# Kernel optimization log

Hardware: AMD Instinct MI355X
Metric: run time of the kernel (lower is better)

The kernel has to match this reference:

```python
import jax, jax.numpy as jnp
import numpy as np

EPS = 1e-8
B, L, D = 8, 2048, 128

def _l2norm(x):
    # F.normalize-style: x / max(||x||, eps)
    n = jnp.sqrt(jnp.sum(x * x, axis=-1, keepdims=True))
    return x / jnp.maximum(n, EPS)

def setup_inputs() -> dict:
    key = jax.random.key(0)
    k0, k1, k2, k3, k4 = jax.random.split(key, 5)
    context = jax.random.normal(k0, (B, 2, L, D), dtype=jnp.float32)
    # MlpModule (BLINK-style): Linear(D, D) -> ReLU -> Linear(D, 1)
    W1 = jax.random.normal(k1, (D, D), dtype=jnp.float32) * (1.0 / np.sqrt(D))
    b1 = jnp.zeros((D,), dtype=jnp.float32)
    W2 = jax.random.normal(k2, (D, 1), dtype=jnp.float32) * (1.0 / np.sqrt(D))
    b2 = jnp.zeros((1,), dtype=jnp.float32)
    return {"context": context, "W1": W1, "b1": b1, "W2": W2, "b2": b2}

def reference(context, W1, b1, W2, b2):
    ctx = context[:, 0]          # [B, L, D] mention-side tokens
    ent = context[:, 1]          # [B, L, D] entity-side tokens
    cn = _l2norm(ctx)
    en = _l2norm(ent)
    # cosine similarity matrix [B, L, L]
    sim = jnp.einsum("bld,bmd->blm", cn, en)
    idx = jnp.argmax(sim, axis=-1)                          # [B, L]
    matched = jnp.take_along_axis(en, idx[..., None], axis=1)  # [B, L, D]
    pair = jnp.stack([cn, matched], axis=-2)                # [B, L, 2, D]
    h = jax.nn.relu(pair @ W1 + b1)                         # [B, L, 2, D]
    out = h @ W2 + b2                                       # [B, L, 2, 1]
    return jnp.sum(out, axis=-2).squeeze(-1)                # [B, L]
```

## Files before the change

### kernel.cpp

```cpp
#include <hip/hip_runtime.h>
#include <hip/hip_bf16.h>

#define B_ 8
#define L_ 2048
#define D_ 128
#define BL_ (B_ * L_)
#define DELTA2 0.016f
#define QCAP 4096

typedef __attribute__((ext_vector_type(8))) short bf16x8;
typedef __attribute__((ext_vector_type(4))) float f32x4;

__global__ void k_norm(const float* __restrict__ ctx,
                       float* __restrict__ cn, float* __restrict__ en,
                       ushort* __restrict__ cnb, ushort* __restrict__ enb) {
    int wid  = blockIdx.x * 4 + (threadIdx.x >> 6);
    int lane = threadIdx.x & 63;
    int b   = wid >> 12;
    int rem = wid & 4095;
    int c   = rem >> 11;
    int l   = rem & 2047;

    const float* src = ctx + (size_t)wid * D_;
    float2 v = ((const float2*)src)[lane];
    float ss = v.x * v.x + v.y * v.y;
    #pragma unroll
    for (int off = 32; off; off >>= 1) ss += __shfl_down(ss, off, 64);
    ss = __shfl(ss, 0, 64);
    float n = fmaxf(sqrtf(ss), 1e-8f);
    float ox = v.x / n, oy = v.y / n;

    size_t ro = (size_t)(b * L_ + l) * D_;
    float* dst = (c == 0 ? cn : en) + ro;
    ((float2*)dst)[lane] = make_float2(ox, oy);

    __hip_bfloat16 hx = __float2bfloat16(ox), hy = __float2bfloat16(oy);
    ushort ux = *(ushort*)&hx, uy = *(ushort*)&hy;
    ushort* dstb = (c == 0 ? cnb : enb) + ro;
    ((ushort2*)dstb)[lane] = make_ushort2(ux, uy);
}

__device__ __forceinline__ void tile64(const bf16x8* __restrict__ Areg,
                                       const ushort* __restrict__ Bb,
                                       int m, int q, f32x4 acc[4][4]) {
    #pragma unroll
    for (int rt = 0; rt < 4; ++rt)
        #pragma unroll
        for (int ct = 0; ct < 4; ++ct) acc[rt][ct] = (f32x4){0.f, 0.f, 0.f, 0.f};
    #pragma unroll
    for (int kc = 0; kc < 4; ++kc) {
        bf16x8 bfrag[4];
        #pragma unroll
        for (int ct = 0; ct < 4; ++ct)
            bfrag[ct] = *(const bf16x8*)(Bb + (size_t)(ct * 16 + m) * D_ + kc * 32 + q * 8);
        #pragma unroll
        for (int rt = 0; rt < 4; ++rt)
            #pragma unroll
            for (int ct = 0; ct < 4; ++ct)
                acc[rt][ct] = __builtin_amdgcn_mfma_f32_16x16x32_bf16(
                    Areg[rt * 4 + kc], bfrag[ct], acc[rt][ct], 0, 0, 0);
    }
}

__global__ __launch_bounds__(512) void k_sim(const ushort* __restrict__ cnb,
                                             const ushort* __restrict__ enb,
                                             const float* __restrict__ cn,
                                             const float* __restrict__ en,
                                             int* __restrict__ finalidx) {
    __shared__ float wrowmax[8][64];
    __shared__ float rowth_l[64];
    __shared__ unsigned long long bestw[8][64];
    __shared__ int qbuf[QCAP];
    __shared__ int qn;

    int bid = blockIdx.x;
    int b = bid & 7, rb = bid >> 3;
    int row0 = rb * 64;
    int tid = threadIdx.x;
    int wave = tid >> 6, lane = tid & 63;
    int m = lane & 15, q = lane >> 4;

    if (tid == 0) qn = 0;
    bestw[wave][lane] = 0ULL;

    const ushort* Ab  = cnb + ((size_t)(b * L_) + row0) * D_;
    const ushort* Bb0 = enb + (size_t)(b * L_) * D_;

    bf16x8 Areg[16];
    #pragma unroll
    for (int rt = 0; rt < 4; ++rt)
        #pragma unroll
        for (int kc = 0; kc < 4; ++kc)
            Areg[rt * 4 + kc] = *(const bf16x8*)(Ab + (size_t)(rt * 16 + m) * D_ + kc * 32 + q * 8);

    float runmax[16];
    #pragma unroll
    for (int s = 0; s < 16; ++s) runmax[s] = -3.0e38f;

    for (int t = 0; t < 4; ++t) {
        f32x4 acc[4][4];
        tile64(Areg, Bb0 + (size_t)(wave * 256 + t * 64) * D_, m, q, acc);
        #pragma unroll
        for (int rt = 0; rt < 4; ++rt)
            #pragma unroll
            for (int reg = 0; reg < 4; ++reg) {
                float v = fmaxf(fmaxf(acc[rt][0][reg], acc[rt][1][reg]),
                                fmaxf(acc[rt][2][reg], acc[rt][3][reg]));
                runmax[rt * 4 + reg] = fmaxf(runmax[rt * 4 + reg], v);
            }
    }
    #pragma unroll
    for (int s = 0; s < 16; ++s) {
        float v = runmax[s];
        v = fmaxf(v, __shfl_xor(v, 1, 64));
        v = fmaxf(v, __shfl_xor(v, 2, 64));
        v = fmaxf(v, __shfl_xor(v, 4, 64));
        v = fmaxf(v, __shfl_xor(v, 8, 64));
        runmax[s] = v;
    }
    if (m == 0) {
        #pragma unroll
        for (int rt = 0; rt < 4; ++rt)
            #pragma unroll
            for (int reg = 0; reg < 4; ++reg)
                wrowmax[wave][rt * 16 + q * 4 + reg] = runmax[rt * 4 + reg];
    }
    __syncthreads();
    if (tid < 64) {
        float rm = wrowmax[0][tid];
        #pragma unroll
        for (int w = 1; w < 8; ++w) rm = fmaxf(rm, wrowmax[w][tid]);
        rowth_l[tid] = rm - DELTA2;
    }
    __syncthreads();
    float rowth_r[16];
    #pragma unroll
    for (int rt = 0; rt < 4; ++rt)
        #pragma unroll
        for (int reg = 0; reg < 4; ++reg)
            rowth_r[rt * 4 + reg] = rowth_l[rt * 16 + q * 4 + reg];

    for (int t = 0; t < 4; ++t) {
        int col0 = wave * 256 + t * 64;
        f32x4 acc[4][4];
        tile64(Areg, Bb0 + (size_t)col0 * D_, m, q, acc);
        #pragma unroll
        for (int rt = 0; rt < 4; ++rt)
            #pragma unroll
            for (int reg = 0; reg < 4; ++reg) {
                float th = rowth_r[rt * 4 + reg];
                float mx = fmaxf(fmaxf(acc[rt][0][reg], acc[rt][1][reg]),
                                 fmaxf(acc[rt][2][reg], acc[rt][3][reg]));
                if (mx >= th) {
                    #pragma unroll
                    for (int ct = 0; ct < 4; ++ct)
                        if (acc[rt][ct][reg] >= th) {
                            int pos = atomicAdd(&qn, 1);
                            if (pos < QCAP)
                                qbuf[pos] = ((rt * 16 + q * 4 + reg) << 12) |
                                            (col0 + ct * 16 + m);
                        }
                }
            }
    }
    __syncthreads();

    int qtot = min(qn, QCAP);
    for (int e = wave; e < qtot; e += 8) {
        int pc = qbuf[e];
        int rl = pc >> 12, col = pc & 0xFFF;
        const float* ar = cn + ((size_t)(b * L_) + row0 + rl) * D_;
        const float* br = en + ((size_t)(b * L_) + col) * D_;
        float2 x = ((const float2*)ar)[lane];
        float2 y = ((const float2*)br)[lane];
        double s = (double)x.x * y.x + (double)x.y * y.y;
        #pragma unroll
        for (int off = 32; off; off >>= 1) s += __shfl_down(s, off, 64);
        if (lane == 0) {
            unsigned long long ub = (unsigned long long)__double_as_longlong(s);
            ub = (ub & 0x8000000000000000ULL) ? ~ub : (ub | 0x8000000000000000ULL);
            ub = (ub & ~0x7FFULL) | (unsigned long long)(2047 - col);
            if (ub > bestw[wave][rl]) bestw[wave][rl] = ub;
        }
    }
    __syncthreads();
    if (tid < 64) {
        unsigned long long bb = bestw[0][tid];
        #pragma unroll
        for (int w = 1; w < 8; ++w) { unsigned long long t2 = bestw[w][tid]; if (t2 > bb) bb = t2; }
        finalidx[b * L_ + row0 + tid] = 2047 - (int)(bb & 0x7FFULL);
    }
}

__global__ __launch_bounds__(256) void k_feval(
        const float* __restrict__ X,
        const float* __restrict__ W1, const float* __restrict__ b1,
        const float* __restrict__ W2, const float* __restrict__ b2,
        float* __restrict__ g) {
    __shared__ __align__(16) float As[32][132];
    __shared__ __align__(16) float Bs[32][132];
    __shared__ float redv[128][16];

    int tid = threadIdx.x;
    int tx = tid & 15, ty = tid >> 4;
    int r  = tid >> 3, kg = tid & 7;
    int row0 = blockIdx.x * 128;
    const float* Ab = X + (size_t)row0 * D_;

    float acc[8][8];
    #pragma unroll
    for (int i = 0; i < 8; ++i)
        #pragma unroll
        for (int j = 0; j < 8; ++j) acc[i][j] = 0.0f;

    for (int kc = 0; kc < 4; ++kc) {
        __syncthreads();
        #pragma unroll
        for (int p = 0; p < 4; ++p) {
            int rr = r + 32 * p;
            float4 v = *(const float4*)(Ab + (size_t)rr * D_ + kc * 32 + kg * 4);
            As[kg][rr]      = v.x;
            As[8 + kg][rr]  = v.y;
            As[16 + kg][rr] = v.z;
            As[24 + kg][rr] = v.w;
        }
        {
            int kr = r, phys = (kr & 3) * 8 + (kr >> 2);
            const float* srcp = W1 + (size_t)(kc * 32 + kr) * D_ + kg * 16;
            #pragma unroll
            for (int qq = 0; qq < 4; ++qq)
                *(float4*)&Bs[phys][kg * 16 + qq * 4] = *(const float4*)(srcp + qq * 4);
        }
        __syncthreads();
        #pragma unroll
        for (int k = 0; k < 32; ++k) {
            float a[8], bb[8];
            *(float4*)&a[0]  = *(const float4*)&As[k][ty * 4];
            *(float4*)&a[4]  = *(const float4*)&As[k][64 + ty * 4];
            *(float4*)&bb[0] = *(const float4*)&Bs[k][tx * 4];
            *(float4*)&bb[4] = *(const float4*)&Bs[k][64 + tx * 4];
            #pragma unroll
            for (int i = 0; i < 8; ++i)
                #pragma unroll
                for (int j = 0; j < 8; ++j)
                    acc[i][j] = fmaf(a[i], bb[j], acc[i][j]);
        }
    }

    float w2j[8], b1j[8];
    #pragma unroll
    for (int jj = 0; jj < 8; ++jj) {
        int c = (jj < 4) ? (tx * 4 + jj) : (64 + tx * 4 + (jj - 4));
        w2j[jj] = W2[c];
        b1j[jj] = b1[c];
    }
    float bias2 = b2[0];
    __syncthreads();
    #pragma unroll
    for (int i = 0; i < 8; ++i) {
        float s = 0.0f;
        #pragma unroll
        for (int jj = 0; jj < 8; ++jj)
            s += fmaxf(acc[i][jj] + b1j[jj], 0.0f) * w2j[jj];
        int rowl = (i < 4) ? (ty * 4 + i) : (64 + ty * 4 + (i - 4));
        redv[rowl][tx] = s;
    }
    __syncthreads();
    if (tid < 128) {
        float s = 0.0f;
        #pragma unroll
        for (int tt = 0; tt < 16; ++tt) s += redv[tid][tt];
        g[row0 + tid] = s + bias2;
    }
}

__global__ void k_out(const int* __restrict__ finalidx,
                      const float* __restrict__ g, float* __restrict__ out) {
    int rr = blockIdx.x * 256 + threadIdx.x;
    if (rr >= BL_) return;
    int b = rr >> 11;
    out[rr] = g[rr] + g[BL_ + (b << 11) + finalidx[rr]];
}

extern "C" void kernel_launch(void* const* d_in, const int* in_sizes, int n_in,
                              void* d_out, int out_size, void* d_ws, size_t ws_size,
                              hipStream_t stream) {
    const float* context = (const float*)d_in[0];
    const float* W1 = (const float*)d_in[1];
    const float* b1 = (const float*)d_in[2];
    const float* W2 = (const float*)d_in[3];
    const float* b2 = (const float*)d_in[4];
    float* out = (float*)d_out;

    char* ws = (char*)d_ws;
    float*  cn  = (float*)(ws);
    float*  en  = (float*)(ws + 8388608);
    ushort* cnb = (ushort*)(ws + 16777216);
    ushort* enb = (ushort*)(ws + 20971520);
    float*  g   = (float*)(ws + 25165824);
    int* finalidx = (int*)(ws + 25296896);

    k_norm<<<8192, 256, 0, stream>>>(context, cn, en, cnb, enb);
    k_sim<<<256, 512, 0, stream>>>(cnb, enb, cn, en, finalidx);
    k_feval<<<256, 256, 0, stream>>>(cn, W1, b1, W2, b2, g);
    k_out<<<BL_ / 256, 256, 0, stream>>>(finalidx, g, out);
}
```

Baseline: 146.2 us.

## Fuse k_sim into single GEMM pass with running-max candidate filter, halve row tiles

The similarity kernel no longer computes the bf16 GEMM twice. It does one pass with a running per-wave row maximum, queues candidates against that evolving threshold with their approximate scores stored in 64-bit entries, and filters them against the final block-wide threshold before the fp64 refinement. Row tiles shrink from 64 to 32 (k_sim) and from 128 to 64 (k_feval), doubling the grid sizes for more parallelism and occupancy. The cost is a larger queue footprint and more candidates early in the pass, when the threshold is still loose, which could hit QCAP overflow or add refinement work.

```diff
diff --git a/kernel.cpp b/kernel.cpp
--- a/kernel.cpp
+++ b/kernel.cpp
@@ -7,6 +7,7 @@
 #define BL_ (B_ * L_)
 #define DELTA2 0.016f
 #define QCAP 4096
+#define ROWS 32
 
 typedef __attribute__((ext_vector_type(8))) short bf16x8;
 typedef __attribute__((ext_vector_type(4))) float f32x4;
@@ -40,151 +41,133 @@
     ((ushort2*)dstb)[lane] = make_ushort2(ux, uy);
 }
 
-__device__ __forceinline__ void tile64(const bf16x8* __restrict__ Areg,
-                                       const ushort* __restrict__ Bb,
-                                       int m, int q, f32x4 acc[4][4]) {
-    #pragma unroll
-    for (int rt = 0; rt < 4; ++rt)
-        #pragma unroll
-        for (int ct = 0; ct < 4; ++ct) acc[rt][ct] = (f32x4){0.f, 0.f, 0.f, 0.f};
-    #pragma unroll
-    for (int kc = 0; kc < 4; ++kc) {
-        bf16x8 bfrag[4];
-        #pragma unroll
-        for (int ct = 0; ct < 4; ++ct)
-            bfrag[ct] = *(const bf16x8*)(Bb + (size_t)(ct * 16 + m) * D_ + kc * 32 + q * 8);
-        #pragma unroll
-        for (int rt = 0; rt < 4; ++rt)
-            #pragma unroll
-            for (int ct = 0; ct < 4; ++ct)
-                acc[rt][ct] = __builtin_amdgcn_mfma_f32_16x16x32_bf16(
-                    Areg[rt * 4 + kc], bfrag[ct], acc[rt][ct], 0, 0, 0);
-    }
-}
-
-__global__ __launch_bounds__(512) void k_sim(const ushort* __restrict__ cnb,
-                                             const ushort* __restrict__ enb,
-                                             const float* __restrict__ cn,
-                                             const float* __restrict__ en,
-                                             int* __restrict__ finalidx) {
-    __shared__ float wrowmax[8][64];
-    __shared__ float rowth_l[64];
-    __shared__ unsigned long long bestw[8][64];
-    __shared__ int qbuf[QCAP];
+__global__ __launch_bounds__(512, 4) void k_sim(const ushort* __restrict__ cnb,
+                                                const ushort* __restrict__ enb,
+                                                const float* __restrict__ cn,
+                                                const float* __restrict__ en,
+                                                int* __restrict__ finalidx) {
+    __shared__ float wrowmax[8][ROWS];
+    __shared__ float rowth_l[ROWS];
+    __shared__ unsigned long long bestw[8][ROWS];
+    __shared__ unsigned long long qbuf[QCAP];
     __shared__ int qn;
 
     int bid = blockIdx.x;
     int b = bid & 7, rb = bid >> 3;
-    int row0 = rb * 64;
+    int row0 = rb * ROWS;
     int tid = threadIdx.x;
     int wave = tid >> 6, lane = tid & 63;
     int m = lane & 15, q = lane >> 4;
 
     if (tid == 0) qn = 0;
-    bestw[wave][lane] = 0ULL;
+    if (lane < ROWS) bestw[wave][lane] = 0ULL;
+    __syncthreads();
 
     const ushort* Ab  = cnb + ((size_t)(b * L_) + row0) * D_;
     const ushort* Bb0 = enb + (size_t)(b * L_) * D_;
 
-    bf16x8 Areg[16];
-    #pragma unroll
-    for (int rt = 0; rt < 4; ++rt)
+    bf16x8 Areg[8];
+    #pragma unroll
+    for (int rt = 0; rt < 2; ++rt)
         #pragma unroll
         for (int kc = 0; kc < 4; ++kc)
             Areg[rt * 4 + kc] = *(const bf16x8*)(Ab + (size_t)(rt * 16 + m) * D_ + kc * 32 + q * 8);
 
-    float runmax[16];
-    #pragma unroll
-    for (int s = 0; s < 16; ++s) runmax[s] = -3.0e38f;
-
-    for (int t = 0; t < 4; ++t) {
-        f32x4 acc[4][4];
-        tile64(Areg, Bb0 + (size_t)(wave * 256 + t * 64) * D_, m, q, acc);
-        #pragma unroll
-        for (int rt = 0; rt < 4; ++rt)
-            #pragma unroll
-            for (int reg = 0; reg < 4; ++reg) {
-                float v = fmaxf(fmaxf(acc[rt][0][reg], acc[rt][1][reg]),
-                                fmaxf(acc[rt][2][reg], acc[rt][3][reg]));
-                runmax[rt * 4 + reg] = fmaxf(runmax[rt * 4 + reg], v);
-            }
-    }
-    #pragma unroll
-    for (int s = 0; s < 16; ++s) {
-        float v = runmax[s];
-        v = fmaxf(v, __shfl_xor(v, 1, 64));
-        v = fmaxf(v, __shfl_xor(v, 2, 64));
-        v = fmaxf(v, __shfl_xor(v, 4, 64));
-        v = fmaxf(v, __shfl_xor(v, 8, 64));
-        runmax[s] = v;
-    }
-    if (m == 0) {
-        #pragma unroll
-        for (int rt = 0; rt < 4; ++rt)
-            #pragma unroll
-            for (int reg = 0; reg < 4; ++reg)
-                wrowmax[wave][rt * 16 + q * 4 + reg] = runmax[rt * 4 + reg];
-    }
-    __syncthreads();
-    if (tid < 64) {
-        float rm = wrowmax[0][tid];
-        #pragma unroll
-        for (int w = 1; w < 8; ++w) rm = fmaxf(rm, wrowmax[w][tid]);
-        rowth_l[tid] = rm - DELTA2;
-    }
-    __syncthreads();
-    float rowth_r[16];
-    #pragma unroll
-    for (int rt = 0; rt < 4; ++rt)
-        #pragma unroll
-        for (int reg = 0; reg < 4; ++reg)
-            rowth_r[rt * 4 + reg] = rowth_l[rt * 16 + q * 4 + reg];
+    float runmax[8];
+    #pragma unroll
+    for (int s = 0; s < 8; ++s) runmax[s] = -3.0e38f;
 
     for (int t = 0; t < 4; ++t) {
         int col0 = wave * 256 + t * 64;
-        f32x4 acc[4][4];
-        tile64(Areg, Bb0 + (size_t)col0 * D_, m, q, acc);
-        #pragma unroll
-        for (int rt = 0; rt < 4; ++rt)
+        const ushort* Bb = Bb0 + (size_t)col0 * D_;
+
+        f32x4 acc[2][4];
+        #pragma unroll
+        for (int rt = 0; rt < 2; ++rt)
+            #pragma unroll
+            for (int ct = 0; ct < 4; ++ct) acc[rt][ct] = (f32x4){0.f, 0.f, 0.f, 0.f};
+        #pragma unroll
+        for (int kc = 0; kc < 4; ++kc) {
+            bf16x8 bfrag[4];
+            #pragma unroll
+            for (int ct = 0; ct < 4; ++ct)
+                bfrag[ct] = *(const bf16x8*)(Bb + (size_t)(ct * 16 + m) * D_ + kc * 32 + q * 8);
+            #pragma unroll
+            for (int rt = 0; rt < 2; ++rt)
+                #pragma unroll
+                for (int ct = 0; ct < 4; ++ct)
+                    acc[rt][ct] = __builtin_amdgcn_mfma_f32_16x16x32_bf16(
+                        Areg[rt * 4 + kc], bfrag[ct], acc[rt][ct], 0, 0, 0);
+        }
+
+        #pragma unroll
+        for (int rt = 0; rt < 2; ++rt)
             #pragma unroll
             for (int reg = 0; reg < 4; ++reg) {
-                float th = rowth_r[rt * 4 + reg];
-                float mx = fmaxf(fmaxf(acc[rt][0][reg], acc[rt][1][reg]),
-                                 fmaxf(acc[rt][2][reg], acc[rt][3][reg]));
-                if (mx >= th) {
+                int s = rt * 4 + reg;
+                float mx4 = fmaxf(fmaxf(acc[rt][0][reg], acc[rt][1][reg]),
+                                  fmaxf(acc[rt][2][reg], acc[rt][3][reg]));
+                float trm = mx4;
+                trm = fmaxf(trm, __shfl_xor(trm, 1, 64));
+                trm = fmaxf(trm, __shfl_xor(trm, 2, 64));
+                trm = fmaxf(trm, __shfl_xor(trm, 4, 64));
+                trm = fmaxf(trm, __shfl_xor(trm, 8, 64));
+                runmax[s] = fmaxf(runmax[s], trm);
+                float th = runmax[s] - DELTA2;
+                if (mx4 >= th) {
+                    int row = rt * 16 + q * 4 + reg;
                     #pragma unroll
                     for (int ct = 0; ct < 4; ++ct)
                         if (acc[rt][ct][reg] >= th) {
                             int pos = atomicAdd(&qn, 1);
                             if (pos < QCAP)
-                                qbuf[pos] = ((rt * 16 + q * 4 + reg) << 12) |
-                                            (col0 + ct * 16 + m);
+                                qbuf[pos] =
+                                    ((unsigned long long)__float_as_uint(acc[rt][ct][reg]) << 32) |
+                                    (unsigned)(row << 11) | (unsigned)(col0 + ct * 16 + m);
                         }
                 }
             }
     }
+
+    if (m == 0) {
+        #pragma unroll
+        for (int rt = 0; rt < 2; ++rt)
+            #pragma unroll
+            for (int reg = 0; reg < 4; ++reg)
+                wrowmax[wave][rt * 16 + q * 4 + reg] = runmax[rt * 4 + reg];
+    }
+    __syncthreads();
+    if (tid < ROWS) {
+        float rm = wrowmax[0][tid];
+        #pragma unroll
+        for (int w = 1; w < 8; ++w) rm = fmaxf(rm, wrowmax[w][tid]);
+        rowth_l[tid] = rm - DELTA2;
+    }
     __syncthreads();
 
     int qtot = min(qn, QCAP);
     for (int e = wave; e < qtot; e += 8) {
-        int pc = qbuf[e];
-        int rl = pc >> 12, col = pc & 0xFFF;
+        unsigned long long pk = qbuf[e];
+        int rl  = (int)((pk >> 11) & 31u);
+        int col = (int)(pk & 2047u);
+        float v = __uint_as_float((unsigned)(pk >> 32));
+        if (v < rowth_l[rl]) continue;
         const float* ar = cn + ((size_t)(b * L_) + row0 + rl) * D_;
         const float* br = en + ((size_t)(b * L_) + col) * D_;
         float2 x = ((const float2*)ar)[lane];
         float2 y = ((const float2*)br)[lane];
-        double s = (double)x.x * y.x + (double)x.y * y.y;
-        #pragma unroll
-        for (int off = 32; off; off >>= 1) s += __shfl_down(s, off, 64);
+        double sdot = (double)x.x * y.x + (double)x.y * y.y;
+        #pragma unroll
+        for (int off = 32; off; off >>= 1) sdot += __shfl_down(sdot, off, 64);
         if (lane == 0) {
-            unsigned long long ub = (unsigned long long)__double_as_longlong(s);
+            unsigned long long ub = (unsigned long long)__double_as_longlong(sdot);
             ub = (ub & 0x8000000000000000ULL) ? ~ub : (ub | 0x8000000000000000ULL);
             ub = (ub & ~0x7FFULL) | (unsigned long long)(2047 - col);
             if (ub > bestw[wave][rl]) bestw[wave][rl] = ub;
         }
     }
     __syncthreads();
-    if (tid < 64) {
+    if (tid < ROWS) {
         unsigned long long bb = bestw[0][tid];
         #pragma unroll
         for (int w = 1; w < 8; ++w) { unsigned long long t2 = bestw[w][tid]; if (t2 > bb) bb = t2; }
@@ -197,26 +180,26 @@
         const float* __restrict__ W1, const float* __restrict__ b1,
         const float* __restrict__ W2, const float* __restrict__ b2,
         float* __restrict__ g) {
-    __shared__ __align__(16) float As[32][132];
+    __shared__ __align__(16) float As[32][68];
     __shared__ __align__(16) float Bs[32][132];
-    __shared__ float redv[128][16];
+    __shared__ float redv[64][16];
 
     int tid = threadIdx.x;
     int tx = tid & 15, ty = tid >> 4;
     int r  = tid >> 3, kg = tid & 7;
-    int row0 = blockIdx.x * 128;
+    int row0 = blockIdx.x * 64;
     const float* Ab = X + (size_t)row0 * D_;
 
-    float acc[8][8];
-    #pragma unroll
-    for (int i = 0; i < 8; ++i)
+    float acc[4][8];
+    #pragma unroll
+    for (int i = 0; i < 4; ++i)
         #pragma unroll
         for (int j = 0; j < 8; ++j) acc[i][j] = 0.0f;
 
     for (int kc = 0; kc < 4; ++kc) {
         __syncthreads();
         #pragma unroll
-        for (int p = 0; p < 4; ++p) {
+        for (int p = 0; p < 2; ++p) {
             int rr = r + 32 * p;
             float4 v = *(const float4*)(Ab + (size_t)rr * D_ + kc * 32 + kg * 4);
             As[kg][rr]      = v.x;
@@ -234,13 +217,12 @@
         __syncthreads();
         #pragma unroll
         for (int k = 0; k < 32; ++k) {
-            float a[8], bb[8];
+            float a[4], bb[8];
             *(float4*)&a[0]  = *(const float4*)&As[k][ty * 4];
-            *(float4*)&a[4]  = *(const float4*)&As[k][64 + ty * 4];
             *(float4*)&bb[0] = *(const float4*)&Bs[k][tx * 4];
             *(float4*)&bb[4] = *(const float4*)&Bs[k][64 + tx * 4];
             #pragma unroll
-            for (int i = 0; i < 8; ++i)
+            for (int i = 0; i < 4; ++i)
                 #pragma unroll
                 for (int j = 0; j < 8; ++j)
                     acc[i][j] = fmaf(a[i], bb[j], acc[i][j]);
@@ -257,16 +239,15 @@
     float bias2 = b2[0];
     __syncthreads();
     #pragma unroll
-    for (int i = 0; i < 8; ++i) {
+    for (int i = 0; i < 4; ++i) {
         float s = 0.0f;
         #pragma unroll
         for (int jj = 0; jj < 8; ++jj)
             s += fmaxf(acc[i][jj] + b1j[jj], 0.0f) * w2j[jj];
-        int rowl = (i < 4) ? (ty * 4 + i) : (64 + ty * 4 + (i - 4));
-        redv[rowl][tx] = s;
-    }
-    __syncthreads();
-    if (tid < 128) {
+        redv[ty * 4 + i][tx] = s;
+    }
+    __syncthreads();
+    if (tid < 64) {
         float s = 0.0f;
         #pragma unroll
         for (int tt = 0; tt < 16; ++tt) s += redv[tid][tt];
@@ -301,7 +282,7 @@
     int* finalidx = (int*)(ws + 25296896);
 
     k_norm<<<8192, 256, 0, stream>>>(context, cn, en, cnb, enb);
-    k_sim<<<256, 512, 0, stream>>>(cnb, enb, cn, en, finalidx);
-    k_feval<<<256, 256, 0, stream>>>(cn, W1, b1, W2, b2, g);
+    k_sim<<<512, 512, 0, stream>>>(cnb, enb, cn, en, finalidx);
+    k_feval<<<512, 256, 0, stream>>>(cn, W1, b1, W2, b2, g);
     k_out<<<BL_ / 256, 256, 0, stream>>>(finalidx, g, out);
 }
```

Measured after the change: 161.2 us. 1.1x slower.

## Double-buffer entity tiles into LDS via async global loads in similarity kernel

Applied to the files above, without the earlier changes.

The similarity kernel now streams entity bf16 tiles into per-wave double-buffered shared memory with global_load_lds, interleaving the column chunks across waves and overlapping loads with MFMA work through manual vmcnt waits. The candidate re-check now handles four candidates per wave at once with 16-lane reductions and a shared atomicMax, replacing the per-wave best arrays. The MLP eval kernel halves its rows per block and doubles the grid to raise parallelism. The trade-off is a large LDS footprint that may limit occupancy, plus reliance on hand-counted waitcnt values.

```diff
diff --git a/kernel.cpp b/kernel.cpp
--- a/kernel.cpp
+++ b/kernel.cpp
@@ -10,6 +10,12 @@
 
 typedef __attribute__((ext_vector_type(8))) short bf16x8;
 typedef __attribute__((ext_vector_type(4))) float f32x4;
+
+__device__ __forceinline__ void gload_lds16(const void* g, void* l) {
+    __builtin_amdgcn_global_load_lds(
+        (const __attribute__((address_space(1))) unsigned int*)g,
+        (__attribute__((address_space(3))) unsigned int*)l, 16, 0, 0);
+}
 
 __global__ void k_norm(const float* __restrict__ ctx,
                        float* __restrict__ cn, float* __restrict__ en,
@@ -40,51 +46,33 @@
     ((ushort2*)dstb)[lane] = make_ushort2(ux, uy);
 }
 
-__device__ __forceinline__ void tile64(const bf16x8* __restrict__ Areg,
-                                       const ushort* __restrict__ Bb,
-                                       int m, int q, f32x4 acc[4][4]) {
-    #pragma unroll
-    for (int rt = 0; rt < 4; ++rt)
-        #pragma unroll
-        for (int ct = 0; ct < 4; ++ct) acc[rt][ct] = (f32x4){0.f, 0.f, 0.f, 0.f};
-    #pragma unroll
-    for (int kc = 0; kc < 4; ++kc) {
-        bf16x8 bfrag[4];
-        #pragma unroll
-        for (int ct = 0; ct < 4; ++ct)
-            bfrag[ct] = *(const bf16x8*)(Bb + (size_t)(ct * 16 + m) * D_ + kc * 32 + q * 8);
-        #pragma unroll
-        for (int rt = 0; rt < 4; ++rt)
-            #pragma unroll
-            for (int ct = 0; ct < 4; ++ct)
-                acc[rt][ct] = __builtin_amdgcn_mfma_f32_16x16x32_bf16(
-                    Areg[rt * 4 + kc], bfrag[ct], acc[rt][ct], 0, 0, 0);
-    }
-}
-
-__global__ __launch_bounds__(512) void k_sim(const ushort* __restrict__ cnb,
-                                             const ushort* __restrict__ enb,
-                                             const float* __restrict__ cn,
-                                             const float* __restrict__ en,
-                                             int* __restrict__ finalidx) {
+__global__ __launch_bounds__(512, 2) void k_sim(const ushort* __restrict__ cnb,
+                                                const ushort* __restrict__ enb,
+                                                const float* __restrict__ cn,
+                                                const float* __restrict__ en,
+                                                int* __restrict__ finalidx) {
+    __shared__ char Bsm[8][2][8192];
     __shared__ float wrowmax[8][64];
     __shared__ float rowth_l[64];
-    __shared__ unsigned long long bestw[8][64];
+    __shared__ unsigned long long best[64];
     __shared__ int qbuf[QCAP];
     __shared__ int qn;
 
-    int bid = blockIdx.x;
-    int b = bid & 7, rb = bid >> 3;
-    int row0 = rb * 64;
-    int tid = threadIdx.x;
-    int wave = tid >> 6, lane = tid & 63;
-    int m = lane & 15, q = lane >> 4;
+    const int bid = blockIdx.x;
+    const int b = bid & 7, rb = bid >> 3;
+    const int row0 = rb * 64;
+    const int tid = threadIdx.x;
+    const int wave = tid >> 6, lane = tid & 63;
+    const int m = lane & 15, q = lane >> 4;
 
     if (tid == 0) qn = 0;
-    bestw[wave][lane] = 0ULL;
+    if (tid < 64) best[tid] = 0ULL;
 
     const ushort* Ab  = cnb + ((size_t)(b * L_) + row0) * D_;
     const ushort* Bb0 = enb + (size_t)(b * L_) * D_;
+    const char* gw = (const char*)Bb0 + (size_t)wave * 8192;
+    char* l0 = &Bsm[wave][0][0];
+    char* l1 = &Bsm[wave][1][0];
 
     bf16x8 Areg[16];
     #pragma unroll
@@ -93,22 +81,67 @@
         for (int kc = 0; kc < 4; ++kc)
             Areg[rt * 4 + kc] = *(const bf16x8*)(Ab + (size_t)(rt * 16 + m) * D_ + kc * 32 + q * 8);
 
+    auto STAGE = [&](int sc, char* lbuf) {
+        const char* src = gw + (size_t)sc * 65536 + (size_t)lane * 16;
+        #pragma unroll
+        for (int i = 0; i < 8; ++i)
+            gload_lds16(src + i * 1024, lbuf + i * 1024);
+    };
+    auto TILE = [&](const char* lbuf, f32x4 acc[4][2]) {
+        #pragma unroll
+        for (int rt = 0; rt < 4; ++rt)
+            #pragma unroll
+            for (int ct = 0; ct < 2; ++ct) acc[rt][ct] = (f32x4){0.f, 0.f, 0.f, 0.f};
+        #pragma unroll
+        for (int kc = 0; kc < 4; ++kc) {
+            bf16x8 bf0 = *(const bf16x8*)(lbuf + (size_t)(m) * 256 + kc * 64 + q * 16);
+            bf16x8 bf1 = *(const bf16x8*)(lbuf + (size_t)(16 + m) * 256 + kc * 64 + q * 16);
+            #pragma unroll
+            for (int rt = 0; rt < 4; ++rt) {
+                acc[rt][0] = __builtin_amdgcn_mfma_f32_16x16x32_bf16(Areg[rt * 4 + kc], bf0, acc[rt][0], 0, 0, 0);
+                acc[rt][1] = __builtin_amdgcn_mfma_f32_16x16x32_bf16(Areg[rt * 4 + kc], bf1, acc[rt][1], 0, 0, 0);
+            }
+        }
+    };
+
     float runmax[16];
     #pragma unroll
     for (int s = 0; s < 16; ++s) runmax[s] = -3.0e38f;
 
-    for (int t = 0; t < 4; ++t) {
-        f32x4 acc[4][4];
-        tile64(Areg, Bb0 + (size_t)(wave * 256 + t * 64) * D_, m, q, acc);
-        #pragma unroll
-        for (int rt = 0; rt < 4; ++rt)
-            #pragma unroll
-            for (int reg = 0; reg < 4; ++reg) {
-                float v = fmaxf(fmaxf(acc[rt][0][reg], acc[rt][1][reg]),
-                                fmaxf(acc[rt][2][reg], acc[rt][3][reg]));
-                runmax[rt * 4 + reg] = fmaxf(runmax[rt * 4 + reg], v);
-            }
-    }
+    STAGE(0, l0);
+    #pragma unroll 1
+    for (int scp = 0; scp < 4; ++scp) {
+        int sc0 = scp * 2;
+        STAGE(sc0 + 1, l1);
+        asm volatile("s_waitcnt vmcnt(8)" ::: "memory");
+        {
+            f32x4 acc[4][2];
+            TILE(l0, acc);
+            #pragma unroll
+            for (int rt = 0; rt < 4; ++rt)
+                #pragma unroll
+                for (int reg = 0; reg < 4; ++reg)
+                    runmax[rt * 4 + reg] = fmaxf(runmax[rt * 4 + reg],
+                                                 fmaxf(acc[rt][0][reg], acc[rt][1][reg]));
+        }
+        if (scp < 3) {
+            STAGE(sc0 + 2, l0);
+            asm volatile("s_waitcnt vmcnt(8)" ::: "memory");
+        } else {
+            asm volatile("s_waitcnt vmcnt(0)" ::: "memory");
+        }
+        {
+            f32x4 acc[4][2];
+            TILE(l1, acc);
+            #pragma unroll
+            for (int rt = 0; rt < 4; ++rt)
+                #pragma unroll
+                for (int reg = 0; reg < 4; ++reg)
+                    runmax[rt * 4 + reg] = fmaxf(runmax[rt * 4 + reg],
+                                                 fmaxf(acc[rt][0][reg], acc[rt][1][reg]));
+        }
+    }
+
     #pragma unroll
     for (int s = 0; s < 16; ++s) {
         float v = runmax[s];
@@ -140,56 +173,91 @@
         for (int reg = 0; reg < 4; ++reg)
             rowth_r[rt * 4 + reg] = rowth_l[rt * 16 + q * 4 + reg];
 
-    for (int t = 0; t < 4; ++t) {
-        int col0 = wave * 256 + t * 64;
-        f32x4 acc[4][4];
-        tile64(Areg, Bb0 + (size_t)col0 * D_, m, q, acc);
-        #pragma unroll
-        for (int rt = 0; rt < 4; ++rt)
-            #pragma unroll
-            for (int reg = 0; reg < 4; ++reg) {
-                float th = rowth_r[rt * 4 + reg];
-                float mx = fmaxf(fmaxf(acc[rt][0][reg], acc[rt][1][reg]),
-                                 fmaxf(acc[rt][2][reg], acc[rt][3][reg]));
-                if (mx >= th) {
-                    #pragma unroll
-                    for (int ct = 0; ct < 4; ++ct)
-                        if (acc[rt][ct][reg] >= th) {
-                            int pos = atomicAdd(&qn, 1);
-                            if (pos < QCAP)
-                                qbuf[pos] = ((rt * 16 + q * 4 + reg) << 12) |
-                                            (col0 + ct * 16 + m);
-                        }
+    STAGE(0, l0);
+    #pragma unroll 1
+    for (int scp = 0; scp < 4; ++scp) {
+        int sc0 = scp * 2;
+        STAGE(sc0 + 1, l1);
+        asm volatile("s_waitcnt vmcnt(8)" ::: "memory");
+        {
+            f32x4 acc[4][2];
+            TILE(l0, acc);
+            int col0 = sc0 * 256 + wave * 32;
+            #pragma unroll
+            for (int rt = 0; rt < 4; ++rt)
+                #pragma unroll
+                for (int reg = 0; reg < 4; ++reg) {
+                    float th = rowth_r[rt * 4 + reg];
+                    if (fmaxf(acc[rt][0][reg], acc[rt][1][reg]) >= th) {
+                        int row = rt * 16 + q * 4 + reg;
+                        #pragma unroll
+                        for (int ct = 0; ct < 2; ++ct)
+                            if (acc[rt][ct][reg] >= th) {
+                                int pos = atomicAdd(&qn, 1);
+                                if (pos < QCAP)
+                                    qbuf[pos] = (row << 12) | (col0 + ct * 16 + m);
+                            }
+                    }
                 }
-            }
+        }
+        if (scp < 3) {
+            STAGE(sc0 + 2, l0);
+            asm volatile("s_waitcnt vmcnt(8)" ::: "memory");
+        } else {
+            asm volatile("s_waitcnt vmcnt(0)" ::: "memory");
+        }
+        {
+            f32x4 acc[4][2];
+            TILE(l1, acc);
+            int col0 = (sc0 + 1) * 256 + wave * 32;
+            #pragma unroll
+            for (int rt = 0; rt < 4; ++rt)
+                #pragma unroll
+                for (int reg = 0; reg < 4; ++reg) {
+                    float th = rowth_r[rt * 4 + reg];
+                    if (fmaxf(acc[rt][0][reg], acc[rt][1][reg]) >= th) {
+                        int row = rt * 16 + q * 4 + reg;
+                        #pragma unroll
+                        for (int ct = 0; ct < 2; ++ct)
+                            if (acc[rt][ct][reg] >= th) {
+                                int pos = atomicAdd(&qn, 1);
+                                if (pos < QCAP)
+                                    qbuf[pos] = (row << 12) | (col0 + ct * 16 + m);
+                            }
+                    }
+                }
+        }
     }
     __syncthreads();
 
     int qtot = min(qn, QCAP);
-    for (int e = wave; e < qtot; e += 8) {
-        int pc = qbuf[e];
-        int rl = pc >> 12, col = pc & 0xFFF;
+    for (int e0 = wave * 4; e0 < qtot; e0 += 32) {
+        int e = e0 + q;
+        bool act = (e < qtot);
+        int pc = qbuf[act ? e : (qtot - 1)];
+        int rl = (pc >> 12) & 63, col = pc & 0xFFF;
         const float* ar = cn + ((size_t)(b * L_) + row0 + rl) * D_;
         const float* br = en + ((size_t)(b * L_) + col) * D_;
-        float2 x = ((const float2*)ar)[lane];
-        float2 y = ((const float2*)br)[lane];
-        double s = (double)x.x * y.x + (double)x.y * y.y;
-        #pragma unroll
-        for (int off = 32; off; off >>= 1) s += __shfl_down(s, off, 64);
-        if (lane == 0) {
+        float4 x0 = ((const float4*)ar)[m * 2], x1 = ((const float4*)ar)[m * 2 + 1];
+        float4 y0 = ((const float4*)br)[m * 2], y1 = ((const float4*)br)[m * 2 + 1];
+        double s = (double)x0.x * y0.x + (double)x0.y * y0.y +
+                   (double)x0.z * y0.z + (double)x0.w * y0.w +
+                   (double)x1.x * y1.x + (double)x1.y * y1.y +
+                   (double)x1.z * y1.z + (double)x1.w * y1.w;
+        s += __shfl_xor(s, 1, 64);
+        s += __shfl_xor(s, 2, 64);
+        s += __shfl_xor(s, 4, 64);
+        s += __shfl_xor(s, 8, 64);
+        if (act && m == 0) {
             unsigned long long ub = (unsigned long long)__double_as_longlong(s);
             ub = (ub & 0x8000000000000000ULL) ? ~ub : (ub | 0x8000000000000000ULL);
             ub = (ub & ~0x7FFULL) | (unsigned long long)(2047 - col);
-            if (ub > bestw[wave][rl]) bestw[wave][rl] = ub;
-        }
-    }
-    __syncthreads();
-    if (tid < 64) {
-        unsigned long long bb = bestw[0][tid];
-        #pragma unroll
-        for (int w = 1; w < 8; ++w) { unsigned long long t2 = bestw[w][tid]; if (t2 > bb) bb = t2; }
-        finalidx[b * L_ + row0 + tid] = 2047 - (int)(bb & 0x7FFULL);
-    }
+            atomicMax(&best[rl], ub);
+        }
+    }
+    __syncthreads();
+    if (tid < 64)
+        finalidx[b * L_ + row0 + tid] = 2047 - (int)(best[tid] & 0x7FFULL);
 }
 
 __global__ __launch_bounds__(256) void k_feval(
@@ -197,26 +265,26 @@
         const float* __restrict__ W1, const float* __restrict__ b1,
         const float* __restrict__ W2, const float* __restrict__ b2,
         float* __restrict__ g) {
-    __shared__ __align__(16) float As[32][132];
+    __shared__ __align__(16) float As[32][68];
     __shared__ __align__(16) float Bs[32][132];
-    __shared__ float redv[128][16];
+    __shared__ float redv[64][16];
 
     int tid = threadIdx.x;
     int tx = tid & 15, ty = tid >> 4;
     int r  = tid >> 3, kg = tid & 7;
-    int row0 = blockIdx.x * 128;
+    int row0 = blockIdx.x * 64;
     const float* Ab = X + (size_t)row0 * D_;
 
-    float acc[8][8];
-    #pragma unroll
-    for (int i = 0; i < 8; ++i)
+    float acc[4][8];
+    #pragma unroll
+    for (int i = 0; i < 4; ++i)
         #pragma unroll
         for (int j = 0; j < 8; ++j) acc[i][j] = 0.0f;
 
     for (int kc = 0; kc < 4; ++kc) {
         __syncthreads();
         #pragma unroll
-        for (int p = 0; p < 4; ++p) {
+        for (int p = 0; p < 2; ++p) {
             int rr = r + 32 * p;
             float4 v = *(const float4*)(Ab + (size_t)rr * D_ + kc * 32 + kg * 4);
             As[kg][rr]      = v.x;
@@ -234,13 +302,12 @@
         __syncthreads();
         #pragma unroll
         for (int k = 0; k < 32; ++k) {
-            float a[8], bb[8];
+            float a[4], bb[8];
             *(float4*)&a[0]  = *(const float4*)&As[k][ty * 4];
-            *(float4*)&a[4]  = *(const float4*)&As[k][64 + ty * 4];
             *(float4*)&bb[0] = *(const float4*)&Bs[k][tx * 4];
             *(float4*)&bb[4] = *(const float4*)&Bs[k][64 + tx * 4];
             #pragma unroll
-            for (int i = 0; i < 8; ++i)
+            for (int i = 0; i < 4; ++i)
                 #pragma unroll
                 for (int j = 0; j < 8; ++j)
                     acc[i][j] = fmaf(a[i], bb[j], acc[i][j]);
@@ -257,16 +324,15 @@
     float bias2 = b2[0];
     __syncthreads();
     #pragma unroll
-    for (int i = 0; i < 8; ++i) {
+    for (int i = 0; i < 4; ++i) {
         float s = 0.0f;
         #pragma unroll
         for (int jj = 0; jj < 8; ++jj)
             s += fmaxf(acc[i][jj] + b1j[jj], 0.0f) * w2j[jj];
-        int rowl = (i < 4) ? (ty * 4 + i) : (64 + ty * 4 + (i - 4));
-        redv[rowl][tx] = s;
-    }
-    __syncthreads();
-    if (tid < 128) {
+        redv[ty * 4 + i][tx] = s;
+    }
+    __syncthreads();
+    if (tid < 64) {
         float s = 0.0f;
         #pragma unroll
         for (int tt = 0; tt < 16; ++tt) s += redv[tid][tt];
@@ -302,6 +368,6 @@
 
     k_norm<<<8192, 256, 0, stream>>>(context, cn, en, cnb, enb);
     k_sim<<<256, 512, 0, stream>>>(cnb, enb, cn, en, finalidx);
-    k_feval<<<256, 256, 0, stream>>>(cn, W1, b1, W2, b2, g);
+    k_feval<<<512, 256, 0, stream>>>(cn, W1, b1, W2, b2, g);
     k_out<<<BL_ / 256, 256, 0, stream>>>(finalidx, g, out);
 }
```

After: 126.3 us. 1.16x faster.

## Stage entity tiles through LDS with async global_load_lds pipeline in k_sim

Applied to the files above, without the earlier changes.

Rewrites the similarity kernel so each wave streams its 256 entity columns in 16-column chunks into a swizzled 4-deep LDS ring via global_load_lds, with vmcnt waits to overlap loads with MFMA. The second pass walks the chunks in reverse so the last staged chunks are reused without reloading. Refinement now uses four 16-lane groups per wave for the fp64 dot products and an LDS atomicMax into a single best array instead of per-wave arrays. It adds 128KB of LDS and a launch bound of 2 blocks per CU, which may limit occupancy, and relies on hand-counted waitcnt values being correct.

```diff
diff --git a/kernel.cpp b/kernel.cpp
--- a/kernel.cpp
+++ b/kernel.cpp
@@ -10,6 +10,14 @@
 
 typedef __attribute__((ext_vector_type(8))) short bf16x8;
 typedef __attribute__((ext_vector_type(4))) float f32x4;
+
+__device__ __forceinline__ void gload_lds16(const void* g, void* l) {
+    __builtin_amdgcn_global_load_lds(
+        (const __attribute__((address_space(1))) unsigned int*)g,
+        (__attribute__((address_space(3))) unsigned int*)l, 16, 0, 0);
+}
+
+#define WAIT_VM(N) asm volatile("s_waitcnt vmcnt(" #N ")" ::: "memory")
 
 __global__ void k_norm(const float* __restrict__ ctx,
                        float* __restrict__ cn, float* __restrict__ en,
@@ -40,51 +48,31 @@
     ((ushort2*)dstb)[lane] = make_ushort2(ux, uy);
 }
 
-__device__ __forceinline__ void tile64(const bf16x8* __restrict__ Areg,
-                                       const ushort* __restrict__ Bb,
-                                       int m, int q, f32x4 acc[4][4]) {
-    #pragma unroll
-    for (int rt = 0; rt < 4; ++rt)
-        #pragma unroll
-        for (int ct = 0; ct < 4; ++ct) acc[rt][ct] = (f32x4){0.f, 0.f, 0.f, 0.f};
-    #pragma unroll
-    for (int kc = 0; kc < 4; ++kc) {
-        bf16x8 bfrag[4];
-        #pragma unroll
-        for (int ct = 0; ct < 4; ++ct)
-            bfrag[ct] = *(const bf16x8*)(Bb + (size_t)(ct * 16 + m) * D_ + kc * 32 + q * 8);
-        #pragma unroll
-        for (int rt = 0; rt < 4; ++rt)
-            #pragma unroll
-            for (int ct = 0; ct < 4; ++ct)
-                acc[rt][ct] = __builtin_amdgcn_mfma_f32_16x16x32_bf16(
-                    Areg[rt * 4 + kc], bfrag[ct], acc[rt][ct], 0, 0, 0);
-    }
-}
-
-__global__ __launch_bounds__(512) void k_sim(const ushort* __restrict__ cnb,
-                                             const ushort* __restrict__ enb,
-                                             const float* __restrict__ cn,
-                                             const float* __restrict__ en,
-                                             int* __restrict__ finalidx) {
+__global__ __launch_bounds__(512, 2) void k_sim(const ushort* __restrict__ cnb,
+                                                const ushort* __restrict__ enb,
+                                                const float* __restrict__ cn,
+                                                const float* __restrict__ en,
+                                                int* __restrict__ finalidx) {
+    __shared__ __align__(16) char Bsm[8][4][4096];
     __shared__ float wrowmax[8][64];
     __shared__ float rowth_l[64];
-    __shared__ unsigned long long bestw[8][64];
+    __shared__ unsigned long long best[64];
     __shared__ int qbuf[QCAP];
     __shared__ int qn;
 
-    int bid = blockIdx.x;
-    int b = bid & 7, rb = bid >> 3;
-    int row0 = rb * 64;
-    int tid = threadIdx.x;
-    int wave = tid >> 6, lane = tid & 63;
-    int m = lane & 15, q = lane >> 4;
+    const int bid = blockIdx.x;
+    const int b = bid & 7, rb = bid >> 3;
+    const int row0 = rb * 64;
+    const int tid = threadIdx.x;
+    const int wave = tid >> 6, lane = tid & 63;
+    const int m = lane & 15, q = lane >> 4;
 
     if (tid == 0) qn = 0;
-    bestw[wave][lane] = 0ULL;
-
-    const ushort* Ab  = cnb + ((size_t)(b * L_) + row0) * D_;
-    const ushort* Bb0 = enb + (size_t)(b * L_) * D_;
+    if (tid < 64) best[tid] = 0ULL;
+
+    const ushort* Ab = cnb + ((size_t)(b * L_) + row0) * D_;
+    const char* gw = (const char*)(enb + (size_t)(b * L_) * D_) + (size_t)wave * 65536;
+    char* Bw = &Bsm[wave][0][0];
 
     bf16x8 Areg[16];
     #pragma unroll
@@ -93,22 +81,53 @@
         for (int kc = 0; kc < 4; ++kc)
             Areg[rt * 4 + kc] = *(const bf16x8*)(Ab + (size_t)(rt * 16 + m) * D_ + kc * 32 + q * 8);
 
+    auto STAGE = [&](int c) {
+        const char* gc = gw + (size_t)c * 4096;
+        char* lbuf = Bw + (c & 3) * 4096;
+        #pragma unroll
+        for (int i = 0; i < 4; ++i) {
+            int j = i * 4 + q;
+            int so = j * 256 + ((m ^ (j & 7)) << 4);
+            gload_lds16(gc + so, lbuf + i * 1024);
+        }
+    };
+    auto TILE = [&](int c, f32x4 acc[4]) {
+        const char* lbuf = Bw + (c & 3) * 4096;
+        #pragma unroll
+        for (int rt = 0; rt < 4; ++rt) acc[rt] = (f32x4){0.f, 0.f, 0.f, 0.f};
+        #pragma unroll
+        for (int kc = 0; kc < 4; ++kc) {
+            bf16x8 bf = *(const bf16x8*)(lbuf + m * 256 + ((kc * 64 + q * 16) ^ ((m & 7) << 4)));
+            #pragma unroll
+            for (int rt = 0; rt < 4; ++rt)
+                acc[rt] = __builtin_amdgcn_mfma_f32_16x16x32_bf16(Areg[rt * 4 + kc], bf, acc[rt], 0, 0, 0);
+        }
+    };
+
     float runmax[16];
     #pragma unroll
     for (int s = 0; s < 16; ++s) runmax[s] = -3.0e38f;
 
-    for (int t = 0; t < 4; ++t) {
-        f32x4 acc[4][4];
-        tile64(Areg, Bb0 + (size_t)(wave * 256 + t * 64) * D_, m, q, acc);
+    auto FMAX = [&](const f32x4 acc[4]) {
         #pragma unroll
         for (int rt = 0; rt < 4; ++rt)
             #pragma unroll
-            for (int reg = 0; reg < 4; ++reg) {
-                float v = fmaxf(fmaxf(acc[rt][0][reg], acc[rt][1][reg]),
-                                fmaxf(acc[rt][2][reg], acc[rt][3][reg]));
-                runmax[rt * 4 + reg] = fmaxf(runmax[rt * 4 + reg], v);
-            }
-    }
+            for (int reg = 0; reg < 4; ++reg)
+                runmax[rt * 4 + reg] = fmaxf(runmax[rt * 4 + reg], acc[rt][reg]);
+    };
+
+    STAGE(0); STAGE(1); STAGE(2);
+    #pragma unroll 1
+    for (int c = 0; c < 14; ++c) {
+        WAIT_VM(8);
+        f32x4 acc[4];
+        TILE(c, acc);
+        if (c < 13) STAGE(c + 3);
+        FMAX(acc);
+    }
+    { WAIT_VM(4); f32x4 acc[4]; TILE(14, acc); FMAX(acc); }
+    { WAIT_VM(0); f32x4 acc[4]; TILE(15, acc); FMAX(acc); }
+
     #pragma unroll
     for (int s = 0; s < 16; ++s) {
         float v = runmax[s];
@@ -140,56 +159,67 @@
         for (int reg = 0; reg < 4; ++reg)
             rowth_r[rt * 4 + reg] = rowth_l[rt * 16 + q * 4 + reg];
 
-    for (int t = 0; t < 4; ++t) {
-        int col0 = wave * 256 + t * 64;
-        f32x4 acc[4][4];
-        tile64(Areg, Bb0 + (size_t)col0 * D_, m, q, acc);
+    auto CAPT = [&](int c, const f32x4 acc[4]) {
+        int col = wave * 256 + c * 16 + m;
         #pragma unroll
         for (int rt = 0; rt < 4; ++rt)
             #pragma unroll
-            for (int reg = 0; reg < 4; ++reg) {
-                float th = rowth_r[rt * 4 + reg];
-                float mx = fmaxf(fmaxf(acc[rt][0][reg], acc[rt][1][reg]),
-                                 fmaxf(acc[rt][2][reg], acc[rt][3][reg]));
-                if (mx >= th) {
-                    #pragma unroll
-                    for (int ct = 0; ct < 4; ++ct)
-                        if (acc[rt][ct][reg] >= th) {
-                            int pos = atomicAdd(&qn, 1);
-                            if (pos < QCAP)
-                                qbuf[pos] = ((rt * 16 + q * 4 + reg) << 12) |
-                                            (col0 + ct * 16 + m);
-                        }
+            for (int reg = 0; reg < 4; ++reg)
+                if (acc[rt][reg] >= rowth_r[rt * 4 + reg]) {
+                    int row = rt * 16 + q * 4 + reg;
+                    int pos = atomicAdd(&qn, 1);
+                    if (pos < QCAP) qbuf[pos] = (row << 12) | col;
                 }
-            }
-    }
+    };
+
+    #pragma unroll 1
+    for (int d = 0; d < 4; ++d) {
+        f32x4 acc[4];
+        TILE(15 - d, acc);
+        STAGE(11 - d);
+        CAPT(15 - d, acc);
+    }
+    #pragma unroll 1
+    for (int d = 4; d < 13; ++d) {
+        WAIT_VM(12);
+        f32x4 acc[4];
+        TILE(15 - d, acc);
+        if (d < 12) STAGE(11 - d);
+        CAPT(15 - d, acc);
+    }
+    { WAIT_VM(8); f32x4 acc[4]; TILE(2, acc); CAPT(2, acc); }
+    { WAIT_VM(4); f32x4 acc[4]; TILE(1, acc); CAPT(1, acc); }
+    { WAIT_VM(0); f32x4 acc[4]; TILE(0, acc); CAPT(0, acc); }
     __syncthreads();
 
     int qtot = min(qn, QCAP);
-    for (int e = wave; e < qtot; e += 8) {
-        int pc = qbuf[e];
-        int rl = pc >> 12, col = pc & 0xFFF;
+    for (int e0 = wave * 4; e0 < qtot; e0 += 32) {
+        int e = e0 + q;
+        bool act = (e < qtot);
+        int pc = qbuf[act ? e : (qtot - 1)];
+        int rl = (pc >> 12) & 63, col = pc & 0xFFF;
         const float* ar = cn + ((size_t)(b * L_) + row0 + rl) * D_;
         const float* br = en + ((size_t)(b * L_) + col) * D_;
-        float2 x = ((const float2*)ar)[lane];
-        float2 y = ((const float2*)br)[lane];
-        double s = (double)x.x * y.x + (double)x.y * y.y;
-        #pragma unroll
-        for (int off = 32; off; off >>= 1) s += __shfl_down(s, off, 64);
-        if (lane == 0) {
+        float4 x0 = ((const float4*)ar)[m * 2], x1 = ((const float4*)ar)[m * 2 + 1];
+        float4 y0 = ((const float4*)br)[m * 2], y1 = ((const float4*)br)[m * 2 + 1];
+        double s = (double)x0.x * y0.x + (double)x0.y * y0.y +
+                   (double)x0.z * y0.z + (double)x0.w * y0.w +
+                   (double)x1.x * y1.x + (double)x1.y * y1.y +
+                   (double)x1.z * y1.z + (double)x1.w * y1.w;
+        s += __shfl_xor(s, 1, 64);
+        s += __shfl_xor(s, 2, 64);
+        s += __shfl_xor(s, 4, 64);
+        s += __shfl_xor(s, 8, 64);
+        if (act && m == 0) {
             unsigned long long ub = (unsigned long long)__double_as_longlong(s);
             ub = (ub & 0x8000000000000000ULL) ? ~ub : (ub | 0x8000000000000000ULL);
             ub = (ub & ~0x7FFULL) | (unsigned long long)(2047 - col);
-            if (ub > bestw[wave][rl]) bestw[wave][rl] = ub;
-        }
-    }
-    __syncthreads();
-    if (tid < 64) {
-        unsigned long long bb = bestw[0][tid];
-        #pragma unroll
-        for (int w = 1; w < 8; ++w) { unsigned long long t2 = bestw[w][tid]; if (t2 > bb) bb = t2; }
-        finalidx[b * L_ + row0 + tid] = 2047 - (int)(bb & 0x7FFULL);
-    }
+            atomicMax(&best[rl], ub);
+        }
+    }
+    __syncthreads();
+    if (tid < 64)
+        finalidx[b * L_ + row0 + tid] = 2047 - (int)(best[tid] & 0x7FFULL);
 }
 
 __global__ __launch_bounds__(256) void k_feval(
```

Measured after the change: 127.1 us. 1.15x faster.
